# Performance work log

Hardware: AMD Instinct MI355X
Metric: run time of the kernel (lower is better)

## Reference

```python
import jax, jax.numpy as jnp
import numpy as np

INPUT_H = 512
INPUT_W = 512
POOL = 5
BN_EPS = 1e-5


def setup_inputs() -> dict:
    key = jax.random.key(0)
    ks = jax.random.split(key, 8)
    B = 16
    c3 = jax.random.normal(ks[0], (B, 512, 64, 64), jnp.float32)
    c4 = jax.random.normal(ks[1], (B, 1024, 32, 32), jnp.float32)
    xy = jax.random.uniform(ks[2], (B, 10, 4), jnp.float32) * 512.0
    # ensure x1<=x2, y1<=y2 like real detector boxes
    boxes = jnp.concatenate([jnp.minimum(xy[..., :2], xy[..., 2:]),
                             jnp.maximum(xy[..., :2], xy[..., 2:])], axis=-1)
    w_conv = jax.random.normal(ks[3], (512, 1536), jnp.float32) * 0.02  # 1x1 conv kernel
    b_conv = jnp.zeros((512,), jnp.float32)
    bn_gamma = jnp.ones((512,), jnp.float32)
    bn_beta = jnp.zeros((512,), jnp.float32)
    bn_mean = jax.random.normal(ks[4], (512,), jnp.float32) * 0.1
    bn_var = jax.random.uniform(ks[5], (512,), jnp.float32) * 0.5 + 0.5
    return {"c3": c3, "c4": c4, "boxes": boxes, "w_conv": w_conv, "b_conv": b_conv,
            "bn_gamma": bn_gamma, "bn_beta": bn_beta, "bn_mean": bn_mean, "bn_var": bn_var}


def _bin_weights(lo, hi, size, nout):
    """Adaptive-avg-pool bin weights over axis of length `size` for crop [lo,hi).
    Returns [nout, size] row-stochastic matrix (same math as AdaptiveAvgPool1d bins)."""
    length = hi - lo
    k = jnp.arange(nout)
    starts = lo + (k * length) // nout                      # floor(k*L/n)
    ends = lo + ((k + 1) * length + nout - 1) // nout        # ceil((k+1)*L/n)
    idx = jnp.arange(size)
    mask = (idx[None, :] >= starts[:, None]) & (idx[None, :] < ends[:, None])
    return mask.astype(jnp.float32) / (ends - starts)[:, None].astype(jnp.float32)


def reference(c3, c4, boxes, w_conv, b_conv, bn_gamma, bn_beta, bn_mean, bn_var):
    B = c3.shape[0]
    c4u = jax.image.resize(c4, (B, c4.shape[1], c4.shape[2] * 2, c4.shape[3] * 2),
                           method='bilinear')
    fused = jnp.concatenate([c3, c4u], axis=1)               # [B,1536,H,W]
    y = jnp.einsum('bchw,oc->bohw', fused, w_conv) + b_conv[None, :, None, None]
    inv = bn_gamma / jnp.sqrt(bn_var + BN_EPS)               # eval-mode BN
    y = y * inv[None, :, None, None] + (bn_beta - bn_mean * inv)[None, :, None, None]
    attr_blob = jax.nn.relu(y)                               # [B,512,H,W]
    H, W = attr_blob.shape[-2:]
    sx = W / INPUT_W
    sy = H / INPUT_H

    def pool_one(feat, box):  # feat [C,H,W], box [4] -> [C,5,5]
        x1 = jnp.clip(jnp.floor(box[0] * sx), 0, W - 1).astype(jnp.int32)
        y1 = jnp.clip(jnp.floor(box[1] * sy), 0, H - 1).astype(jnp.int32)
        x2 = jnp.clip(jnp.ceil(box[2] * sx), 0, W - 1).astype(jnp.int32)
        y2 = jnp.clip(jnp.ceil(box[3] * sy), 0, H - 1).astype(jnp.int32)
        x2 = jnp.where(x2 <= x1, jnp.minimum(x1 + 1, W), x2)
        y2 = jnp.where(y2 <= y1, jnp.minimum(y1 + 1, H), y2)
        wy = _bin_weights(y1, y2, H, POOL)                   # [5,H]
        wx = _bin_weights(x1, x2, W, POOL)                   # [5,W]
        return jnp.einsum('ph,chw,qw->cpq', wy, feat, wx)

    obj_blob = jax.vmap(lambda f, bx: jax.vmap(lambda b: pool_one(f, b))(bx))(attr_blob, boxes)
    return boxes, obj_blob  # ([B,10,4], [B,10,512,5,5])
```

## Files before the change

### kernel.cpp

```cpp
#include <hip/hip_runtime.h>
#include <stdint.h>

#define FH 64
#define FW 64
#define CIN 1536
#define C3C 512
#define C4C 1024
#define COUT 512
#define BATCH 16
#define NPIX 4096
#define NBOX 10
#define MPAD 256
#define KT128 12

#define NB_FU 12288
#define NB_P  4000
#define NB_W  768
#define NB_BN 2
#define NB_CP 3
#define NB_TOT (NB_FU + NB_P + NB_W + NB_BN + NB_CP)

typedef float v4f __attribute__((ext_vector_type(4)));
typedef long  v2l __attribute__((ext_vector_type(2)));

#define GLOAD_LDS16(g, l) __builtin_amdgcn_global_load_lds( \
    (const __attribute__((address_space(1))) void*)(g),     \
    (__attribute__((address_space(3))) void*)(l), 16, 0, 0)

#define BARRIER() asm volatile("s_barrier" ::: "memory")

__device__ __forceinline__ uint32_t pack4_fp8(float a, float b, float c, float d) {
    int lo = __builtin_amdgcn_cvt_pk_fp8_f32(a, b, 0, false);
    int v  = __builtin_amdgcn_cvt_pk_fp8_f32(c, d, lo, true);
    return (uint32_t)v;
}
__device__ __forceinline__ unsigned char f32_to_fp8(float a) {
    return (unsigned char)(__builtin_amdgcn_cvt_pk_fp8_f32(a, a, 0, false) & 0xff);
}


__global__ __launch_bounds__(256) void mega_pre(
        const float* __restrict__ c3, const float* __restrict__ c4,
        const float* __restrict__ boxes,
        const float* __restrict__ w_conv, const float* __restrict__ b_conv,
        const float* __restrict__ bng, const float* __restrict__ bnb,
        const float* __restrict__ bnm, const float* __restrict__ bnv,
        unsigned char* __restrict__ fusedT, unsigned char* __restrict__ P,
        unsigned char* __restrict__ w8,
        float* __restrict__ scale, float* __restrict__ shift,
        float* __restrict__ out) {
    __shared__ uint32_t lds[64 * 36];
    const int bid = blockIdx.x;
    const int t   = threadIdx.x;

    if (bid < NB_FU) {
        int ct = bid % 12;
        int rest = bid / 12;
        int y  = rest & 63;
        int b  = rest >> 6;
        int pg = t & 15;
        int cq = t >> 4;

        #pragma unroll
        for (int r = 0; r < 2; ++r) {
            int cquad = cq + 16 * r;
            float vv[4][4];
            if (ct < 4) {
                int ch = ct * 128 + 4 * cquad;
                const float* src = c3 + (((size_t)(b * C3C + ch) * FH + y) * FW) + 4 * pg;
                #pragma unroll
                for (int k = 0; k < 4; ++k) {
                    float4 f = *(const float4*)(src + (size_t)k * (FH * FW));
                    vv[k][0] = f.x; vv[k][1] = f.y; vv[k][2] = f.z; vv[k][3] = f.w;
                }
            } else {
                int ch = ct * 128 - 512 + 4 * cquad;
                int jy = y >> 1;
                int jyB = min(max(jy + ((y & 1) ? 1 : -1), 0), 31);
                const float* base = c4 + (size_t)(b * C4C + ch) * 1024;
                #pragma unroll
                for (int k = 0; k < 4; ++k) {
                    const float* pc = base + (size_t)k * 1024;
                    float2 f0 = *(const float2*)(pc + jy * 32 + 2 * pg);
                    float2 f1 = *(const float2*)(pc + jyB * 32 + 2 * pg);
                    float rbA = 0.75f * f0.x + 0.25f * f1.x;
                    float rbB = 0.75f * f0.y + 0.25f * f1.y;
                    float rbm = __shfl_up(rbB, 1, 16);
                    float rbp = __shfl_down(rbA, 1, 16);
                    if (pg == 0)  rbm = rbA;
                    if (pg == 15) rbp = rbB;
                    vv[k][0] = 0.75f * rbA + 0.25f * rbm;
                    vv[k][1] = 0.75f * rbA + 0.25f * rbB;
                    vv[k][2] = 0.75f * rbB + 0.25f * rbA;
                    vv[k][3] = 0.75f * rbB + 0.25f * rbp;
                }
            }
            #pragma unroll
            for (int i = 0; i < 4; ++i) {
                int px = 4 * pg + i;
                lds[px * 36 + 4 * ((cquad >> 2) ^ ((px >> 1) & 7)) + (cquad & 3)] =
                    pack4_fp8(vv[0][i], vv[1][i], vv[2][i], vv[3][i]);
            }
        }
        __syncthreads();
        int g = t & 7;
        #pragma unroll
        for (int rr2 = 0; rr2 < 2; ++rr2) {
            int px = (t >> 3) + 32 * rr2;
            uint4 w = *(const uint4*)(&lds[px * 36 + 4 * (g ^ ((px >> 1) & 7))]);
            unsigned char* dst = fusedT + ((size_t)b * NPIX + y * FW + px) * CIN + ct * 128;
            int pos0 = ((2 * g) & 3) * 32 + (g >> 1) * 8;
            int pos1 = ((2 * g + 1) & 3) * 32 + (g >> 1) * 8;
            *(uint2*)(dst + pos0) = make_uint2(w.x, w.y);
            *(uint2*)(dst + pos1) = make_uint2(w.z, w.w);
        }
    } else if (bid < NB_FU + NB_P) {
        int id  = bid - NB_FU;
        int br  = id % 160;
        int m25 = id / 160;
        int b   = br / NBOX;
        int m   = (br % NBOX) * 25 + m25;
        int p   = m25 / 5, q = m25 % 5;
        int y   = t >> 2;
        int x0  = (t & 3) * 16;
        const float* bx = boxes + (size_t)br * 4;
        int x1 = min(max((int)floorf(bx[0] * 0.125f), 0), 63);
        int y1 = min(max((int)floorf(bx[1] * 0.125f), 0), 63);
        int x2 = min(max((int)ceilf (bx[2] * 0.125f), 0), 63);
        int y2 = min(max((int)ceilf (bx[3] * 0.125f), 0), 63);
        if (x2 <= x1) x2 = min(x1 + 1, 64);
        if (y2 <= y1) y2 = min(y1 + 1, 64);
        int Lx = x2 - x1, Ly = y2 - y1;
        int sx = x1 + (q * Lx) / 5;
        int ex = x1 + ((q + 1) * Lx + 4) / 5;
        int sy = y1 + (p * Ly) / 5;
        int ey = y1 + ((p + 1) * Ly + 4) / 5;
        float wyv  = (y >= sy && y < ey) ? 1.0f / (float)(ey - sy) : 0.0f;
        float pval = 64.0f * wyv / (float)(ex - sx);
        float v[16];
        #pragma unroll
        for (int i = 0; i < 16; ++i) {
            int xi = x0 + i;
            v[i] = (xi >= sx && xi < ex) ? pval : 0.0f;
        }
        uint4 w;
        w.x = pack4_fp8(v[0],  v[1],  v[2],  v[3]);
        w.y = pack4_fp8(v[4],  v[5],  v[6],  v[7]);
        w.z = pack4_fp8(v[8],  v[9],  v[10], v[11]);
        w.w = pack4_fp8(v[12], v[13], v[14], v[15]);
        *(uint4*)(P + ((size_t)b * MPAD + m) * NPIX + y * FW + x0) = w;
    } else if (bid < NB_FU + NB_P + NB_W) {
        int i = (bid - NB_FU - NB_P) * 256 + t;
        if (i < COUT * CIN / 4) {
            float4 f = *(const float4*)(w_conv + i * 4);
            uint32_t v = pack4_fp8(f.x * 16.0f, f.y * 16.0f, f.z * 16.0f, f.w * 16.0f);
            int c0 = (i * 4) % CIN;
            int o  = (i * 4) / CIN;
            int k7 = c0 & 127;
            int pos = ((k7 >> 3) & 3) * 32 + (k7 >> 5) * 8 + (k7 & 7);
            *(uint32_t*)(w8 + (size_t)o * CIN + (c0 & ~127) + pos) = v;
        }
    } else if (bid < NB_FU + NB_P + NB_W + NB_BN) {
        int o = (bid - NB_FU - NB_P - NB_W) * 256 + t;
        if (o < COUT) {
            float inv = bng[o] / sqrtf(bnv[o] + 1e-5f);
            scale[o] = inv * 0.0625f;
            shift[o] = bnb[o] + inv * (b_conv[o] - bnm[o]);
        }
    } else {
        int i = (bid - NB_FU - NB_P - NB_W - NB_BN) * 256 + t;
        if (i < 640) out[i] = boxes[i];
    }
}

__global__ __launch_bounds__(512, 2) void gemm_bn_relu(
        const unsigned char* __restrict__ w8,
        const unsigned char* __restrict__ fusedT,
        const float* __restrict__ scale, const float* __restrict__ shift,
        unsigned char* __restrict__ attr) {
    __shared__ __align__(16) unsigned char lds_a[2][32768];
    __shared__ __align__(16) unsigned char lds_b[2][32768];
    const int t  = threadIdx.x;
    const int n0 = blockIdx.x * 256;
    const int o0 = blockIdx.y * 256;
    const int b  = blockIdx.z;
    const int wave = t >> 6, lane = t & 63;
    const int wm = wave & 1, wn = wave >> 1;
    const int quad = lane >> 4, l16 = lane & 15;
    const int cp0 = (((quad << 1) ^ (l16 & 7)) << 4);
    const int cp1 = cp0 ^ 16;
    const unsigned char* fb = fusedT + (size_t)b * NPIX * CIN;

    const int rr = t >> 3;
    const int cg = (t & 7) ^ (rr & 7);
    const unsigned char* gA = w8 + (size_t)(o0 + rr) * CIN + cg * 16;
    const unsigned char* gB = fb + (size_t)(n0 + rr) * CIN + cg * 16;

#define SA(u, kt, d) GLOAD_LDS16(gA + (size_t)(u) * (64 * CIN) + (kt) * 128, \
                                 &lds_a[d][(u) * 8192 + t * 16])
#define SB(u, kt, d) GLOAD_LDS16(gB + (size_t)(u) * (64 * CIN) + (kt) * 128, \
                                 &lds_b[d][(u) * 8192 + t * 16])
#define RAV(d, ph, i, cp) (*(const v2l*)(&lds_a[d][((wm * 128 + (ph) * 64 + (i) * 16 + l16) << 7) + (cp)]))
#define RBV(d, j, cp)     (*(const v2l*)(&lds_b[d][((wn * 64 + (j) * 16 + l16) << 7) + (cp)]))

    v4f acc[8][4];
    #pragma unroll
    for (int i = 0; i < 8; ++i)
        #pragma unroll
        for (int j = 0; j < 4; ++j) acc[i][j] = (v4f)0.0f;

    SA(0, 0, 0); SA(1, 0, 0); SA(2, 0, 0); SA(3, 0, 0);
    SB(0, 0, 0); SB(1, 0, 0); SB(2, 0, 0); SB(3, 0, 0);
    SA(0, 1, 1); SA(2, 1, 1); SB(0, 1, 1); SB(1, 1, 1); SB(2, 1, 1); SB(3, 1, 1);
    asm volatile("s_waitcnt vmcnt(6)" ::: "memory");
    BARRIER();

    v2l ah0[4], ah1[4], bh0[4], bh1[4];

    for (int kt = 0; kt < KT128; ++kt) {
        const int cur = kt & 1, nxt = cur ^ 1;

        #pragma unroll
        for (int i = 0; i < 4; ++i) { ah0[i] = RAV(cur, 0, i, cp0); ah1[i] = RAV(cur, 0, i, cp1); }
        #pragma unroll
        for (int j = 0; j < 4; ++j) { bh0[j] = RBV(cur, j, cp0); bh1[j] = RBV(cur, j, cp1); }
        if (kt > 0 && kt + 1 < KT128) {
            SA(0, kt + 1, nxt); SA(2, kt + 1, nxt);
            SB(0, kt + 1, nxt); SB(1, kt + 1, nxt);
            SB(2, kt + 1, nxt); SB(3, kt + 1, nxt);
        }
        __builtin_amdgcn_s_setprio(1);
        #pragma unroll
        for (int s = 0; s < 2; ++s)
            #pragma unroll
            for (int i = 0; i < 4; ++i)
                #pragma unroll
                for (int j = 0; j < 4; ++j)
                    acc[i][j] = __builtin_amdgcn_mfma_f32_16x16x32_fp8_fp8(ah0[i][s], bh0[j][s], acc[i][j], 0, 0, 0);
        #pragma unroll
        for (int s = 0; s < 2; ++s)
            #pragma unroll
            for (int i = 0; i < 4; ++i)
                #pragma unroll
                for (int j = 0; j < 4; ++j)
                    acc[i][j] = __builtin_amdgcn_mfma_f32_16x16x32_fp8_fp8(ah1[i][s], bh1[j][s], acc[i][j], 0, 0, 0);
        __builtin_amdgcn_s_setprio(0);
        if (kt + 1 < KT128) { asm volatile("s_waitcnt vmcnt(6)" ::: "memory"); }
        else               { asm volatile("s_waitcnt vmcnt(0)" ::: "memory"); }
        BARRIER();

        #pragma unroll
        for (int i = 0; i < 4; ++i) { ah0[i] = RAV(cur, 1, i, cp0); ah1[i] = RAV(cur, 1, i, cp1); }
        if (kt + 1 < KT128) { SA(1, kt + 1, nxt); SA(3, kt + 1, nxt); }
        __builtin_amdgcn_s_setprio(1);
        #pragma unroll
        for (int s = 0; s < 2; ++s)
            #pragma unroll
            for (int i = 0; i < 4; ++i)
                #pragma unroll
                for (int j = 0; j < 4; ++j)
                    acc[4 + i][j] = __builtin_amdgcn_mfma_f32_16x16x32_fp8_fp8(ah0[i][s], bh0[j][s], acc[4 + i][j], 0, 0, 0);
        #pragma unroll
        for (int s = 0; s < 2; ++s)
            #pragma unroll
            for (int i = 0; i < 4; ++i)
                #pragma unroll
                for (int j = 0; j < 4; ++j)
                    acc[4 + i][j] = __builtin_amdgcn_mfma_f32_16x16x32_fp8_fp8(ah1[i][s], bh1[j][s], acc[4 + i][j], 0, 0, 0);
        __builtin_amdgcn_s_setprio(0);
        if (kt + 1 < KT128) { asm volatile("s_waitcnt vmcnt(2)" ::: "memory"); }
        BARRIER();
    }

    unsigned char* ab = attr + (size_t)b * COUT * NPIX;
    #pragma unroll
    for (int a = 0; a < 8; ++a) {
        int obase = o0 + wm * 128 + (a >> 2) * 64 + (a & 3) * 16 + quad * 4;
        #pragma unroll
        for (int r = 0; r < 4; ++r) {
            int oo = obase + r;
            float sc = scale[oo], sh = shift[oo];
            #pragma unroll
            for (int j = 0; j < 4; ++j) {
                int n = n0 + wn * 64 + j * 16 + l16;
                float v = fmaxf(acc[a][j][r] * sc + sh, 0.0f);
                ab[(size_t)oo * NPIX + n] = f32_to_fp8(v);
            }
        }
    }
#undef SA
#undef SB
#undef RAV
#undef RBV
}

__global__ __launch_bounds__(256) void pool_fused(
        const unsigned char* __restrict__ P,
        const unsigned char* __restrict__ attr,
        float* __restrict__ out) {
    __shared__ __align__(16) unsigned char lds_a[128 * 64];
    __shared__ __align__(16) unsigned char lds_b[128 * 64];
    int t  = threadIdx.x;
    int m0 = blockIdx.x * 128;
    int c0 = blockIdx.y * 128;
    int b  = blockIdx.z;
    int wave = t >> 6, lane = t & 63;
    int wm = wave & 1, wn = wave >> 1;
    int quad = lane >> 4, l16 = lane & 15;
    const unsigned char* Pb = P + (size_t)b * MPAD * NPIX;
    const unsigned char* ab = attr + (size_t)b * COUT * NPIX;

    v4f acc[4][4];
    #pragma unroll
    for (int i = 0; i < 4; ++i)
        #pragma unroll
        for (int j = 0; j < 4; ++j) acc[i][j] = (v4f)0.0f;

    int row = t >> 2;
    int cg  = (t & 3) ^ ((row >> 1) & 3);
    const unsigned char* ga0 = Pb + (size_t)(m0 + row) * NPIX + cg * 16;
    const unsigned char* ga1 = Pb + (size_t)(m0 + row + 64) * NPIX + cg * 16;
    const unsigned char* gb0 = ab + (size_t)(c0 + row) * NPIX + cg * 16;
    const unsigned char* gb1 = ab + (size_t)(c0 + row + 64) * NPIX + cg * 16;
    unsigned char* la0 = lds_a + t * 16;
    unsigned char* la1 = lds_a + 4096 + t * 16;
    unsigned char* lb0 = lds_b + t * 16;
    unsigned char* lb1 = lds_b + 4096 + t * 16;

    int ra[4], rb[4];
    #pragma unroll
    for (int i = 0; i < 4; ++i) { ra[i] = wm * 64 + i * 16 + l16; rb[i] = wn * 64 + i * 16 + l16; }
    int q2 = quad >> 1, q1 = (quad & 1) * 8;

    for (int kt = 0; kt < NPIX / 64; ++kt) {
        __syncthreads();
        GLOAD_LDS16(ga0, la0);
        GLOAD_LDS16(ga1, la1);
        GLOAD_LDS16(gb0, lb0);
        GLOAD_LDS16(gb1, lb1);
        ga0 += 64; ga1 += 64; gb0 += 64; gb1 += 64;
        __syncthreads();

        #pragma unroll
        for (int s = 0; s < 2; ++s) {
            long af[4], bf[4];
            #pragma unroll
            for (int i = 0; i < 4; ++i) {
                int pa = (2 * s + q2) ^ ((ra[i] >> 1) & 3);
                af[i] = *(const long*)(lds_a + ra[i] * 64 + pa * 16 + q1);
                int pb = (2 * s + q2) ^ ((rb[i] >> 1) & 3);
                bf[i] = *(const long*)(lds_b + rb[i] * 64 + pb * 16 + q1);
            }
            #pragma unroll
            for (int i = 0; i < 4; ++i)
                #pragma unroll
                for (int j = 0; j < 4; ++j)
                    acc[i][j] = __builtin_amdgcn_mfma_f32_16x16x32_fp8_fp8(af[i], bf[j], acc[i][j], 0, 0, 0);
        }
    }

    #pragma unroll
    for (int i = 0; i < 4; ++i) {
        #pragma unroll
        for (int r = 0; r < 4; ++r) {
            int mrow = m0 + wm * 64 + i * 16 + quad * 4 + r;
            if (mrow < 250) {
                int box = mrow / 25, bin = mrow - box * 25;
                float* ob = out + 640 + ((size_t)(b * NBOX + box) * COUT) * 25 + bin;
                #pragma unroll
                for (int j = 0; j < 4; ++j) {
                    int c = c0 + wn * 64 + j * 16 + l16;
                    ob[(size_t)c * 25] = acc[i][j][r] * 0.015625f;
                }
            }
        }
    }
}

extern "C" void kernel_launch(void* const* d_in, const int* in_sizes, int n_in,
                              void* d_out, int out_size, void* d_ws, size_t ws_size,
                              hipStream_t stream) {
    const float* c3     = (const float*)d_in[0];
    const float* c4     = (const float*)d_in[1];
    const float* boxes  = (const float*)d_in[2];
    const float* w_conv = (const float*)d_in[3];
    const float* b_conv = (const float*)d_in[4];
    const float* bng    = (const float*)d_in[5];
    const float* bnb    = (const float*)d_in[6];
    const float* bnm    = (const float*)d_in[7];
    const float* bnv    = (const float*)d_in[8];
    float* out = (float*)d_out;

    char* ws = (char*)d_ws;
    unsigned char* fusedT = (unsigned char*)ws;
    unsigned char* P      = (unsigned char*)(ws + 100663296);
    unsigned char* w8     = (unsigned char*)(ws + 117440512);
    float*         scale  = (float*)(ws + 118226944);
    float*         shift  = (float*)(ws + 118228992);
    unsigned char* attr   = (unsigned char*)(ws + 118231040);

    mega_pre<<<NB_TOT, 256, 0, stream>>>(c3, c4, boxes, w_conv, b_conv,
                                         bng, bnb, bnm, bnv,
                                         fusedT, P, w8, scale, shift, out);
    gemm_bn_relu<<<dim3(16, 2, 16), 512, 0, stream>>>(w8, fusedT, scale, shift, attr);
    pool_fused<<<dim3(2, 4, 16), 256, 0, stream>>>(P, attr, out);
    (void)in_sizes; (void)n_in; (void)out_size; (void)ws_size;
}
```

Measured before the change: 395.5 us.

## Split-K the pooling GEMM with a reduce pass and process two rows per prep block

The pooling GEMM previously ran only 128 blocks, each looping over all 4096 pixels. It now splits K into 4 segments, giving 512 blocks that write fp32 partials, and a new reduce kernel sums them and scatters into the output layout. Separately, the fused-input prep blocks now handle two output rows each, halving the block count. For the upsampled c4 path this lets both rows share one loaded center row. The costs are an extra kernel launch, about 32 MB of partial-sum traffic, and higher register and LDS use in the prep blocks.

```diff
diff --git a/kernel.cpp b/kernel.cpp
--- a/kernel.cpp
+++ b/kernel.cpp
@@ -13,7 +13,7 @@
 #define MPAD 256
 #define KT128 12
 
-#define NB_FU 12288
+#define NB_FU 6144
 #define NB_P  4000
 #define NB_W  768
 #define NB_BN 2
@@ -49,71 +49,108 @@
         unsigned char* __restrict__ w8,
         float* __restrict__ scale, float* __restrict__ shift,
         float* __restrict__ out) {
-    __shared__ uint32_t lds[64 * 36];
+    __shared__ uint32_t lds[2 * 64 * 36];
     const int bid = blockIdx.x;
     const int t   = threadIdx.x;
 
     if (bid < NB_FU) {
         int ct = bid % 12;
         int rest = bid / 12;
-        int y  = rest & 63;
-        int b  = rest >> 6;
+        int yj = rest & 31;
+        int b  = rest >> 5;
         int pg = t & 15;
         int cq = t >> 4;
 
-        #pragma unroll
-        for (int r = 0; r < 2; ++r) {
-            int cquad = cq + 16 * r;
-            float vv[4][4];
-            if (ct < 4) {
-                int ch = ct * 128 + 4 * cquad;
-                const float* src = c3 + (((size_t)(b * C3C + ch) * FH + y) * FW) + 4 * pg;
+        if (ct < 4) {
+            float4 f3[2][2][4];
+            #pragma unroll
+            for (int yi = 0; yi < 2; ++yi)
+                #pragma unroll
+                for (int r = 0; r < 2; ++r) {
+                    int ch = ct * 128 + 4 * (cq + 16 * r);
+                    const float* src = c3 + (((size_t)(b * C3C + ch) * FH + (2 * yj + yi)) * FW) + 4 * pg;
+                    #pragma unroll
+                    for (int k = 0; k < 4; ++k)
+                        f3[yi][r][k] = *(const float4*)(src + (size_t)k * (FH * FW));
+                }
+            #pragma unroll
+            for (int yi = 0; yi < 2; ++yi)
+                #pragma unroll
+                for (int r = 0; r < 2; ++r) {
+                    int cquad = cq + 16 * r;
+                    float vv[4][4];
+                    #pragma unroll
+                    for (int k = 0; k < 4; ++k) {
+                        vv[k][0] = f3[yi][r][k].x; vv[k][1] = f3[yi][r][k].y;
+                        vv[k][2] = f3[yi][r][k].z; vv[k][3] = f3[yi][r][k].w;
+                    }
+                    #pragma unroll
+                    for (int i = 0; i < 4; ++i) {
+                        int px = 4 * pg + i;
+                        lds[yi * 2304 + px * 36 + 4 * ((cquad >> 2) ^ ((px >> 1) & 7)) + (cquad & 3)] =
+                            pack4_fp8(vv[0][i], vv[1][i], vv[2][i], vv[3][i]);
+                    }
+                }
+        } else {
+            int jy  = yj;
+            int rm1 = max(jy - 1, 0);
+            int rp1 = min(jy + 1, 31);
+            float2 g0[2][4], gm[2][4], gp[2][4];
+            #pragma unroll
+            for (int r = 0; r < 2; ++r) {
+                int ch = ct * 128 - 512 + 4 * (cq + 16 * r);
+                const float* base = c4 + (size_t)(b * C4C + ch) * 1024;
                 #pragma unroll
                 for (int k = 0; k < 4; ++k) {
-                    float4 f = *(const float4*)(src + (size_t)k * (FH * FW));
-                    vv[k][0] = f.x; vv[k][1] = f.y; vv[k][2] = f.z; vv[k][3] = f.w;
-                }
-            } else {
-                int ch = ct * 128 - 512 + 4 * cquad;
-                int jy = y >> 1;
-                int jyB = min(max(jy + ((y & 1) ? 1 : -1), 0), 31);
-                const float* base = c4 + (size_t)(b * C4C + ch) * 1024;
-                #pragma unroll
-                for (int k = 0; k < 4; ++k) {
-                    const float* pc = base + (size_t)k * 1024;
-                    float2 f0 = *(const float2*)(pc + jy * 32 + 2 * pg);
-                    float2 f1 = *(const float2*)(pc + jyB * 32 + 2 * pg);
-                    float rbA = 0.75f * f0.x + 0.25f * f1.x;
-                    float rbB = 0.75f * f0.y + 0.25f * f1.y;
-                    float rbm = __shfl_up(rbB, 1, 16);
-                    float rbp = __shfl_down(rbA, 1, 16);
-                    if (pg == 0)  rbm = rbA;
-                    if (pg == 15) rbp = rbB;
-                    vv[k][0] = 0.75f * rbA + 0.25f * rbm;
-                    vv[k][1] = 0.75f * rbA + 0.25f * rbB;
-                    vv[k][2] = 0.75f * rbB + 0.25f * rbA;
-                    vv[k][3] = 0.75f * rbB + 0.25f * rbp;
+                    const float* pc = base + (size_t)k * 1024 + 2 * pg;
+                    g0[r][k] = *(const float2*)(pc + jy * 32);
+                    gm[r][k] = *(const float2*)(pc + rm1 * 32);
+                    gp[r][k] = *(const float2*)(pc + rp1 * 32);
                 }
             }
             #pragma unroll
-            for (int i = 0; i < 4; ++i) {
-                int px = 4 * pg + i;
-                lds[px * 36 + 4 * ((cquad >> 2) ^ ((px >> 1) & 7)) + (cquad & 3)] =
-                    pack4_fp8(vv[0][i], vv[1][i], vv[2][i], vv[3][i]);
-            }
+            for (int yi = 0; yi < 2; ++yi)
+                #pragma unroll
+                for (int r = 0; r < 2; ++r) {
+                    int cquad = cq + 16 * r;
+                    float vv[4][4];
+                    #pragma unroll
+                    for (int k = 0; k < 4; ++k) {
+                        float2 f0 = g0[r][k];
+                        float2 f1 = yi ? gp[r][k] : gm[r][k];
+                        float rbA = 0.75f * f0.x + 0.25f * f1.x;
+                        float rbB = 0.75f * f0.y + 0.25f * f1.y;
+                        float rbm = __shfl_up(rbB, 1, 16);
+                        float rbp = __shfl_down(rbA, 1, 16);
+                        if (pg == 0)  rbm = rbA;
+                        if (pg == 15) rbp = rbB;
+                        vv[k][0] = 0.75f * rbA + 0.25f * rbm;
+                        vv[k][1] = 0.75f * rbA + 0.25f * rbB;
+                        vv[k][2] = 0.75f * rbB + 0.25f * rbA;
+                        vv[k][3] = 0.75f * rbB + 0.25f * rbp;
+                    }
+                    #pragma unroll
+                    for (int i = 0; i < 4; ++i) {
+                        int px = 4 * pg + i;
+                        lds[yi * 2304 + px * 36 + 4 * ((cquad >> 2) ^ ((px >> 1) & 7)) + (cquad & 3)] =
+                            pack4_fp8(vv[0][i], vv[1][i], vv[2][i], vv[3][i]);
+                    }
+                }
         }
         __syncthreads();
         int g = t & 7;
         #pragma unroll
-        for (int rr2 = 0; rr2 < 2; ++rr2) {
-            int px = (t >> 3) + 32 * rr2;
-            uint4 w = *(const uint4*)(&lds[px * 36 + 4 * (g ^ ((px >> 1) & 7))]);
-            unsigned char* dst = fusedT + ((size_t)b * NPIX + y * FW + px) * CIN + ct * 128;
-            int pos0 = ((2 * g) & 3) * 32 + (g >> 1) * 8;
-            int pos1 = ((2 * g + 1) & 3) * 32 + (g >> 1) * 8;
-            *(uint2*)(dst + pos0) = make_uint2(w.x, w.y);
-            *(uint2*)(dst + pos1) = make_uint2(w.z, w.w);
-        }
+        for (int yi = 0; yi < 2; ++yi)
+            #pragma unroll
+            for (int rr2 = 0; rr2 < 2; ++rr2) {
+                int px = (t >> 3) + 32 * rr2;
+                uint4 w = *(const uint4*)(&lds[yi * 2304 + px * 36 + 4 * (g ^ ((px >> 1) & 7))]);
+                unsigned char* dst = fusedT + ((size_t)b * NPIX + (2 * yj + yi) * FW + px) * CIN + ct * 128;
+                int pos0 = ((2 * g) & 3) * 32 + (g >> 1) * 8;
+                int pos1 = ((2 * g + 1) & 3) * 32 + (g >> 1) * 8;
+                *(uint2*)(dst + pos0) = make_uint2(w.x, w.y);
+                *(uint2*)(dst + pos1) = make_uint2(w.z, w.w);
+            }
     } else if (bid < NB_FU + NB_P) {
         int id  = bid - NB_FU;
         int br  = id % 160;
@@ -294,21 +331,22 @@
 #undef RBV
 }
 
-__global__ __launch_bounds__(256) void pool_fused(
+__global__ __launch_bounds__(256) void pool_gemm(
         const unsigned char* __restrict__ P,
         const unsigned char* __restrict__ attr,
-        float* __restrict__ out) {
+        float* __restrict__ part2) {
     __shared__ __align__(16) unsigned char lds_a[128 * 64];
     __shared__ __align__(16) unsigned char lds_b[128 * 64];
     int t  = threadIdx.x;
     int m0 = blockIdx.x * 128;
-    int c0 = blockIdx.y * 128;
+    int c0 = (blockIdx.y & 3) * 128;
+    int seg = blockIdx.y >> 2;
     int b  = blockIdx.z;
     int wave = t >> 6, lane = t & 63;
     int wm = wave & 1, wn = wave >> 1;
     int quad = lane >> 4, l16 = lane & 15;
-    const unsigned char* Pb = P + (size_t)b * MPAD * NPIX;
-    const unsigned char* ab = attr + (size_t)b * COUT * NPIX;
+    const unsigned char* Pb = P + (size_t)b * MPAD * NPIX + seg * 1024;
+    const unsigned char* ab = attr + (size_t)b * COUT * NPIX + seg * 1024;
 
     v4f acc[4][4];
     #pragma unroll
@@ -332,7 +370,7 @@
     for (int i = 0; i < 4; ++i) { ra[i] = wm * 64 + i * 16 + l16; rb[i] = wn * 64 + i * 16 + l16; }
     int q2 = quad >> 1, q1 = (quad & 1) * 8;
 
-    for (int kt = 0; kt < NPIX / 64; ++kt) {
+    for (int kt = 0; kt < 1024 / 64; ++kt) {
         __syncthreads();
         GLOAD_LDS16(ga0, la0);
         GLOAD_LDS16(ga1, la1);
@@ -359,22 +397,32 @@
         }
     }
 
+    float* pp = part2 + (((size_t)seg * BATCH + b) * MPAD) * COUT;
     #pragma unroll
     for (int i = 0; i < 4; ++i) {
         #pragma unroll
         for (int r = 0; r < 4; ++r) {
             int mrow = m0 + wm * 64 + i * 16 + quad * 4 + r;
-            if (mrow < 250) {
-                int box = mrow / 25, bin = mrow - box * 25;
-                float* ob = out + 640 + ((size_t)(b * NBOX + box) * COUT) * 25 + bin;
-                #pragma unroll
-                for (int j = 0; j < 4; ++j) {
-                    int c = c0 + wn * 64 + j * 16 + l16;
-                    ob[(size_t)c * 25] = acc[i][j][r] * 0.015625f;
-                }
+            #pragma unroll
+            for (int j = 0; j < 4; ++j) {
+                int c = c0 + wn * 64 + j * 16 + l16;
+                pp[(size_t)mrow * COUT + c] = acc[i][j][r];
             }
         }
     }
+}
+
+__global__ __launch_bounds__(256) void pool_reduce(const float* __restrict__ part2,
+                                                   float* __restrict__ out) {
+    const size_t SEG = (size_t)BATCH * MPAD * COUT;
+    int i = blockIdx.x * 256 + threadIdx.x;
+    int c = i & (COUT - 1);
+    int m = (i >> 9) & (MPAD - 1);
+    int b = i >> 17;
+    if (m >= 250) return;
+    float s = part2[i] + part2[i + SEG] + part2[i + 2 * SEG] + part2[i + 3 * SEG];
+    int box = m / 25, bin = m - box * 25;
+    out[640 + ((size_t)(b * NBOX + box) * COUT + c) * 25 + bin] = s * 0.015625f;
 }
 
 extern "C" void kernel_launch(void* const* d_in, const int* in_sizes, int n_in,
@@ -394,15 +442,17 @@
     char* ws = (char*)d_ws;
     unsigned char* fusedT = (unsigned char*)ws;
     unsigned char* P      = (unsigned char*)(ws + 100663296);
-    unsigned char* w8     = (unsigned char*)(ws + 117440512);
-    float*         scale  = (float*)(ws + 118226944);
-    float*         shift  = (float*)(ws + 118228992);
-    unsigned char* attr   = (unsigned char*)(ws + 118231040);
+    float*         part2  = (float*)(ws + 117440512);
+    unsigned char* w8     = (unsigned char*)(ws + 150994944);
+    float*         scale  = (float*)(ws + 151781376);
+    float*         shift  = (float*)(ws + 151783424);
+    unsigned char* attr   = (unsigned char*)(ws + 151785472);
 
     mega_pre<<<NB_TOT, 256, 0, stream>>>(c3, c4, boxes, w_conv, b_conv,
                                          bng, bnb, bnm, bnv,
                                          fusedT, P, w8, scale, shift, out);
     gemm_bn_relu<<<dim3(16, 2, 16), 512, 0, stream>>>(w8, fusedT, scale, shift, attr);
-    pool_fused<<<dim3(2, 4, 16), 256, 0, stream>>>(P, attr, out);
+    pool_gemm<<<dim3(2, 16, 16), 256, 0, stream>>>(P, attr, part2);
+    pool_reduce<<<(BATCH * MPAD * COUT) / 256, 256, 0, stream>>>(part2, out);
     (void)in_sizes; (void)n_in; (void)out_size; (void)ws_size;
 }
```

After: 385.0 us. 1.03x faster.

## Split pooling GEMM along K into four segments with a separate reduce kernel

Applied to the files above, without the earlier changes.

The pooling GEMM previously launched only 128 blocks, each looping over all 4096 pixels. It now splits K into four 1024-pixel segments, launching 512 blocks that write fp32 partials to a new workspace buffer. A new reduce kernel sums the four partials, applies the 1/64 scaling and scatters into the output layout. Separately, the fused-transpose stores are remapped so each thread writes one 16-byte chunk instead of two 8-byte scattered writes, with the LDS permutation changed to match. The split costs an extra launch and about 32 MB of partial-sum traffic.

```diff
diff --git a/kernel.cpp b/kernel.cpp
--- a/kernel.cpp
+++ b/kernel.cpp
@@ -95,10 +95,11 @@
                     vv[k][3] = 0.75f * rbB + 0.25f * rbp;
                 }
             }
+            int wp = ((cquad >> 1) & 3) * 8 + (cquad >> 3) * 2 + (cquad & 1);
             #pragma unroll
             for (int i = 0; i < 4; ++i) {
                 int px = 4 * pg + i;
-                lds[px * 36 + 4 * ((cquad >> 2) ^ ((px >> 1) & 7)) + (cquad & 3)] =
+                lds[px * 36 + 4 * ((wp >> 2) ^ ((px >> 1) & 7)) + (wp & 3)] =
                     pack4_fp8(vv[0][i], vv[1][i], vv[2][i], vv[3][i]);
             }
         }
@@ -108,11 +109,7 @@
         for (int rr2 = 0; rr2 < 2; ++rr2) {
             int px = (t >> 3) + 32 * rr2;
             uint4 w = *(const uint4*)(&lds[px * 36 + 4 * (g ^ ((px >> 1) & 7))]);
-            unsigned char* dst = fusedT + ((size_t)b * NPIX + y * FW + px) * CIN + ct * 128;
-            int pos0 = ((2 * g) & 3) * 32 + (g >> 1) * 8;
-            int pos1 = ((2 * g + 1) & 3) * 32 + (g >> 1) * 8;
-            *(uint2*)(dst + pos0) = make_uint2(w.x, w.y);
-            *(uint2*)(dst + pos1) = make_uint2(w.z, w.w);
+            *(uint4*)(fusedT + ((size_t)b * NPIX + y * FW + px) * CIN + ct * 128 + g * 16) = w;
         }
     } else if (bid < NB_FU + NB_P) {
         int id  = bid - NB_FU;
@@ -294,21 +291,22 @@
 #undef RBV
 }
 
-__global__ __launch_bounds__(256) void pool_fused(
+__global__ __launch_bounds__(256) void pool_gemm(
         const unsigned char* __restrict__ P,
         const unsigned char* __restrict__ attr,
-        float* __restrict__ out) {
+        float* __restrict__ part2) {
     __shared__ __align__(16) unsigned char lds_a[128 * 64];
     __shared__ __align__(16) unsigned char lds_b[128 * 64];
     int t  = threadIdx.x;
     int m0 = blockIdx.x * 128;
-    int c0 = blockIdx.y * 128;
+    int c0 = (blockIdx.y & 3) * 128;
+    int seg = blockIdx.y >> 2;
     int b  = blockIdx.z;
     int wave = t >> 6, lane = t & 63;
     int wm = wave & 1, wn = wave >> 1;
     int quad = lane >> 4, l16 = lane & 15;
-    const unsigned char* Pb = P + (size_t)b * MPAD * NPIX;
-    const unsigned char* ab = attr + (size_t)b * COUT * NPIX;
+    const unsigned char* Pb = P + (size_t)b * MPAD * NPIX + seg * 1024;
+    const unsigned char* ab = attr + (size_t)b * COUT * NPIX + seg * 1024;
 
     v4f acc[4][4];
     #pragma unroll
@@ -332,7 +330,7 @@
     for (int i = 0; i < 4; ++i) { ra[i] = wm * 64 + i * 16 + l16; rb[i] = wn * 64 + i * 16 + l16; }
     int q2 = quad >> 1, q1 = (quad & 1) * 8;
 
-    for (int kt = 0; kt < NPIX / 64; ++kt) {
+    for (int kt = 0; kt < 1024 / 64; ++kt) {
         __syncthreads();
         GLOAD_LDS16(ga0, la0);
         GLOAD_LDS16(ga1, la1);
@@ -359,22 +357,32 @@
         }
     }
 
+    float* pp = part2 + (((size_t)seg * BATCH + b) * MPAD) * COUT;
     #pragma unroll
     for (int i = 0; i < 4; ++i) {
         #pragma unroll
         for (int r = 0; r < 4; ++r) {
             int mrow = m0 + wm * 64 + i * 16 + quad * 4 + r;
-            if (mrow < 250) {
-                int box = mrow / 25, bin = mrow - box * 25;
-                float* ob = out + 640 + ((size_t)(b * NBOX + box) * COUT) * 25 + bin;
-                #pragma unroll
-                for (int j = 0; j < 4; ++j) {
-                    int c = c0 + wn * 64 + j * 16 + l16;
-                    ob[(size_t)c * 25] = acc[i][j][r] * 0.015625f;
-                }
+            #pragma unroll
+            for (int j = 0; j < 4; ++j) {
+                int c = c0 + wn * 64 + j * 16 + l16;
+                pp[(size_t)mrow * COUT + c] = acc[i][j][r];
             }
         }
     }
+}
+
+__global__ __launch_bounds__(256) void pool_reduce(const float* __restrict__ part2,
+                                                   float* __restrict__ out) {
+    const size_t SEG = (size_t)BATCH * MPAD * COUT;
+    int i = blockIdx.x * 256 + threadIdx.x;
+    int c = i & (COUT - 1);
+    int m = (i >> 9) & (MPAD - 1);
+    int b = i >> 17;
+    if (m >= 250) return;
+    float s = part2[i] + part2[i + SEG] + part2[i + 2 * SEG] + part2[i + 3 * SEG];
+    int box = m / 25, bin = m - box * 25;
+    out[640 + ((size_t)(b * NBOX + box) * COUT + c) * 25 + bin] = s * 0.015625f;
 }
 
 extern "C" void kernel_launch(void* const* d_in, const int* in_sizes, int n_in,
@@ -394,15 +402,17 @@
     char* ws = (char*)d_ws;
     unsigned char* fusedT = (unsigned char*)ws;
     unsigned char* P      = (unsigned char*)(ws + 100663296);
-    unsigned char* w8     = (unsigned char*)(ws + 117440512);
-    float*         scale  = (float*)(ws + 118226944);
-    float*         shift  = (float*)(ws + 118228992);
-    unsigned char* attr   = (unsigned char*)(ws + 118231040);
+    float*         part2  = (float*)(ws + 117440512);
+    unsigned char* w8     = (unsigned char*)(ws + 150994944);
+    float*         scale  = (float*)(ws + 151781376);
+    float*         shift  = (float*)(ws + 151783424);
+    unsigned char* attr   = (unsigned char*)(ws + 151785472);
 
     mega_pre<<<NB_TOT, 256, 0, stream>>>(c3, c4, boxes, w_conv, b_conv,
                                          bng, bnb, bnm, bnv,
                                          fusedT, P, w8, scale, shift, out);
     gemm_bn_relu<<<dim3(16, 2, 16), 512, 0, stream>>>(w8, fusedT, scale, shift, attr);
-    pool_fused<<<dim3(2, 4, 16), 256, 0, stream>>>(P, attr, out);
+    pool_gemm<<<dim3(2, 16, 16), 256, 0, stream>>>(P, attr, part2);
+    pool_reduce<<<(BATCH * MPAD * COUT) / 256, 256, 0, stream>>>(part2, out);
     (void)in_sizes; (void)n_in; (void)out_size; (void)ws_size;
 }
```

Measured after the change: 379.5 us. 4.1% less time.
